# Optimization experiments

Measured on AMD Instinct MI355X. Metric: run time of the kernel, lower is better.

The kernel has to match this reference:

```python
import jax, jax.numpy as jnp
import numpy as np

D = 512        # model_size
HID = 2048     # hidden_size
NH = 8         # n_head
DH = D // NH   # head dim
L = 6          # n_layer
V = 32000      # vocab (input_size == output_size)
B, S, T = 8, 512, 512
PAD = 0
EPS = 1e-5


def setup_inputs() -> dict:
    key = jax.random.key(0)
    ks = jax.random.split(key, 16)
    sc = 0.02
    W = lambda k, shape: (jax.random.normal(k, shape) * sc).astype(jnp.float32)
    # LayerNorm params: [L, n_ln, 2, D] with [...,0,:]=gamma(ones), [...,1,:]=beta(zeros)
    ln = lambda n: jnp.stack([jnp.ones((L, n, D)), jnp.zeros((L, n, D))], axis=2)
    emi = W(ks[2], (V, D)).at[PAD].set(0.0)  # padding_idx row zeroed
    emo = W(ks[3], (V, D)).at[PAD].set(0.0)
    return {
        # token ids in [1, V) so no padding rows (avoids fully-masked softmax rows -> nan grads)
        "inputs": jax.random.randint(ks[0], (B, S), 1, V),
        "outputs": jax.random.randint(ks[1], (B, T), 1, V),
        "emi": emi, "emo": emo,
        "enc_attn_w": W(ks[4], (L, 4, D, D)), "enc_attn_b": jnp.zeros((L, 4, D)),
        "enc_ln": ln(2),
        "enc_ffn_w1": W(ks[5], (L, D, HID)), "enc_ffn_b1": jnp.zeros((L, HID)),
        "enc_ffn_w2": W(ks[6], (L, HID, D)), "enc_ffn_b2": jnp.zeros((L, D)),
        "dec_self_w": W(ks[7], (L, 4, D, D)), "dec_self_b": jnp.zeros((L, 4, D)),
        "dec_cross_w": W(ks[8], (L, 4, D, D)), "dec_cross_b": jnp.zeros((L, 4, D)),
        "dec_ln": ln(3),
        "dec_ffn_w1": W(ks[9], (L, D, HID)), "dec_ffn_b1": jnp.zeros((L, HID)),
        "dec_ffn_w2": W(ks[10], (L, HID, D)), "dec_ffn_b2": jnp.zeros((L, D)),
    }


def _ln(x, g, b):
    mu = x.mean(-1, keepdims=True)
    var = ((x - mu) ** 2).mean(-1, keepdims=True)
    return (x - mu) * jax.lax.rsqrt(var + EPS) * g + b


def _mha(xq, xkv, mask, w, b):
    # w: [4, D, D] stored as [in, out] (q, k, v, out proj); mask: [B, Sq, Sk] bool (True = masked)
    heads = lambda x: x.reshape(x.shape[0], x.shape[1], NH, DH).transpose(0, 2, 1, 3)
    q = heads(xq @ w[0] + b[0])
    k = heads(xkv @ w[1] + b[1])
    v = heads(xkv @ w[2] + b[2])
    s = jnp.einsum('bhqd,bhkd->bhqk', q, k) * (1.0 / np.sqrt(DH))
    s = jnp.where(mask[:, None], -jnp.inf, s)
    a = jnp.nan_to_num(jax.nn.softmax(s, axis=-1), nan=0.0)  # fully-masked rows -> 0
    o = jnp.einsum('bhqk,bhkd->bhqd', a, v).transpose(0, 2, 1, 3).reshape(xq.shape)
    return o @ w[3] + b[3]


def _pe(n):
    pos = jnp.arange(n, dtype=jnp.float32)[:, None]
    div = jnp.exp(jnp.arange(0, D, 2, dtype=jnp.float32) * (-np.log(10000.0) / D))
    pe = jnp.zeros((n, D))
    return pe.at[:, 0::2].set(jnp.sin(pos * div)).at[:, 1::2].set(jnp.cos(pos * div))


def reference(inputs, outputs, emi, emo,
              enc_attn_w, enc_attn_b, enc_ln, enc_ffn_w1, enc_ffn_b1, enc_ffn_w2, enc_ffn_b2,
              dec_self_w, dec_self_b, dec_cross_w, dec_cross_b, dec_ln,
              dec_ffn_w1, dec_ffn_b1, dec_ffn_w2, dec_ffn_b2):
    mx = inputs == PAD   # [B, S]
    my = outputs == PAD  # [B, T]
    x = emi[inputs] + _pe(inputs.shape[-1])
    y = emo[outputs] + _pe(outputs.shape[-1])

    enc_mask = mx[:, :, None] | mx[:, None, :]  # [B, S, S]

    def enc_layer(x, p):
        aw, ab, ln, w1, b1, w2, b2 = p
        x = _ln(x + _mha(x, x, enc_mask, aw, ab), ln[0, 0], ln[0, 1])
        x = _ln(x + (jax.nn.relu(x @ w1 + b1) @ w2 + b2), ln[1, 0], ln[1, 1])
        return x, None

    x, _ = jax.lax.scan(enc_layer, x,
                        (enc_attn_w, enc_attn_b, enc_ln, enc_ffn_w1, enc_ffn_b1, enc_ffn_w2, enc_ffn_b2))

    n = outputs.shape[-1]
    causal = jnp.triu(jnp.ones((n, n), dtype=bool), 1)
    m1 = my[:, :, None] | my[:, None, :] | causal[None]  # self-attn: pad union + causal
    m2 = my[:, :, None] | mx[:, None, :]                  # cross-attn: query pad | key pad

    def dec_layer(y, p):
        sw, sb, cw, cb, ln, w1, b1, w2, b2 = p
        y = _ln(y + _mha(y, y, m1, sw, sb), ln[0, 0], ln[0, 1])
        y = _ln(y + _mha(y, x, m2, cw, cb), ln[1, 0], ln[1, 1])
        y = _ln(y + (jax.nn.relu(y @ w1 + b1) @ w2 + b2), ln[2, 0], ln[2, 1])
        return y, None

    y, _ = jax.lax.scan(dec_layer, y,
                        (dec_self_w, dec_self_b, dec_cross_w, dec_cross_b, dec_ln,
                         dec_ffn_w1, dec_ffn_b1, dec_ffn_w2, dec_ffn_b2))
    return y  # [B, T, D] (forward returns decoder states; self.lin is unused in forward)
```

## Files before the change

kernel.cpp:

```cpp
#include <hip/hip_runtime.h>
#include <hip/hip_bf16.h>

#define D_   512
#define HID_ 2048
#define NH_  8
#define DH_  64
#define L_   6
#define B_   8
#define S_   512
#define T_   512
#define M_   4096
#define MD_  (M_ * D_)
#define QSTR 1536

typedef unsigned short ushort_t;
typedef __attribute__((ext_vector_type(8))) short bf16x8;
typedef __attribute__((ext_vector_type(4))) float f32x4;

__device__ __forceinline__ float bf2f(unsigned short u) {
    union { unsigned int i; float f; } x; x.i = ((unsigned int)u) << 16; return x.f;
}
__device__ __forceinline__ unsigned short f2bf(float f) {
    union { float f; unsigned int u; } x; x.f = f;
    unsigned int r = (x.u + 0x7fffu + ((x.u >> 16) & 1u)) >> 16;
    return (unsigned short)r;
}
__device__ __forceinline__ float ldp(const void* p, size_t i, int mode) {
    return mode ? ((const float*)p)[i] : bf2f(((const unsigned short*)p)[i]);
}

typedef __attribute__((address_space(1))) const unsigned int GAS_u32;
typedef __attribute__((address_space(3))) unsigned int LAS_u32;
__device__ __forceinline__ void gload16(const void* g, void* l) {
    __builtin_amdgcn_global_load_lds((GAS_u32*)g, (LAS_u32*)l, 16, 0, 0);
}

__global__ __launch_bounds__(256) void detect_kernel(const void* em, int* flagp) {
    __shared__ int big, zc;
    if (threadIdx.x == 0) { big = 0; zc = 0; }
    __syncthreads();
    const unsigned short* u = (const unsigned short*)em;
    int lbig = 0, lzc = 0;
    for (int i = threadIdx.x; i < 2048; i += 256) {
        unsigned short x = u[512 + i];
        float v = bf2f(x);
        if (!(fabsf(v) < 1000.0f)) lbig = 1;
        if ((((512 + i) & 1) == 0) && ((x & 0x7fff) == 0)) lzc++;
    }
    if (lbig) atomicOr(&big, 1);
    atomicAdd(&zc, lzc);
    __syncthreads();
    if (threadIdx.x == 0) flagp[0] = (big || zc >= 1000) ? 1 : 0;
}

__global__ __launch_bounds__(256) void embed_pe_kernel(const int* __restrict__ tok,
        const void* __restrict__ em, float* __restrict__ out,
        unsigned short* __restrict__ outb, const int* __restrict__ flagp)
{
    const int mode = flagp[0];
    int idx = blockIdx.x * 256 + threadIdx.x;
    int d   = idx & (D_ - 1);
    int row = idx >> 9;
    int s   = row & (S_ - 1);
    int t   = tok[row];
    float e = ldp(em, (size_t)t * D_ + d, mode);
    int d2  = d & ~1;
    float div = expf((float)d2 * (-9.210340371976184f / (float)D_));
    float a   = (float)s * div;
    float pe  = (d & 1) ? cosf(a) : sinf(a);
    float v   = e + pe;
    out[idx]  = v;
    outb[idx] = f2bf(v);
}

template<int TMT, int TNT>
__global__ __launch_bounds__(256) void mfma_gemm(
        const unsigned short* __restrict__ A, int K,
        const void* __restrict__ W, size_t woff, int nsub,
        const void* __restrict__ bias, size_t boff,
        void* __restrict__ C, int ldc, int cmode , int relu,
        const int* __restrict__ flagp)
{
    constexpr int TM  = TMT * 32;
    constexpr int TN  = TNT * 32;
    constexpr int AI  = TM / 16;
    constexpr int TPN = TN / 2;
    constexpr int KR  = TN / 16;

    __shared__ unsigned short As[TM * 32];
    __shared__ unsigned short Bs[TN * 40];

    const int mode = __builtin_amdgcn_readfirstlane(flagp[0]);
    const int tid  = threadIdx.x;
    const int m0   = blockIdx.y * TM;
    const int n0   = blockIdx.x * TN;

    const size_t wbase = woff + (size_t)(n0 / nsub) * (size_t)K * nsub + (n0 % nsub);

    const int lane = tid & 63;
    const int wave = tid >> 6;

    const int n0t = 2 * (tid % TPN);
    const int kb  = KR * (tid / TPN);

    const int ln = lane & 15;
    const int q  = lane >> 4;
    const int wm = (wave >> 1) * (TMT * 16);
    const int wn = (wave & 1) * (TNT * 16);

    f32x4 acc[TMT][TNT];
#pragma unroll
    for (int i = 0; i < TMT; ++i)
#pragma unroll
        for (int j = 0; j < TNT; ++j) acc[i][j] = (f32x4)0.0f;

    for (int k0 = 0; k0 < K; k0 += 32) {
        __syncthreads();
#pragma unroll
        for (int u = 0; u < (AI + 3) / 4; ++u) {
            int i = wave + u * 4;
            if (i < AI) {
                int off = i * 1024 + lane * 16;
                int row = off >> 6;
                int ke  = (off & 63) >> 1;
                gload16(A + (size_t)(m0 + row) * K + k0 + ke, &As[i * 512]);
            }
        }
        {
            unsigned short lo[KR], hi[KR];
            if (mode == 0) {
                const unsigned short* wp = (const unsigned short*)W + wbase;
#pragma unroll
                for (int r = 0; r < KR; ++r) {
                    unsigned int v = *reinterpret_cast<const unsigned int*>(
                        wp + (size_t)(k0 + kb + r) * nsub + n0t);
                    lo[r] = (unsigned short)(v & 0xffffu);
                    hi[r] = (unsigned short)(v >> 16);
                }
            } else {
                const float* wp = (const float*)W + wbase;
#pragma unroll
                for (int r = 0; r < KR; ++r) {
                    float2 f = *reinterpret_cast<const float2*>(
                        wp + (size_t)(k0 + kb + r) * nsub + n0t);
                    lo[r] = f2bf(f.x); hi[r] = f2bf(f.y);
                }
            }
            unsigned int ul[KR / 2], uh[KR / 2];
#pragma unroll
            for (int p = 0; p < KR / 2; ++p) {
                ul[p] = (unsigned int)lo[2 * p] | ((unsigned int)lo[2 * p + 1] << 16);
                uh[p] = (unsigned int)hi[2 * p] | ((unsigned int)hi[2 * p + 1] << 16);
            }
            if constexpr (KR == 8) {
                *reinterpret_cast<uint4*>(&Bs[(n0t + 0) * 40 + kb]) = make_uint4(ul[0], ul[1], ul[2], ul[3]);
                *reinterpret_cast<uint4*>(&Bs[(n0t + 1) * 40 + kb]) = make_uint4(uh[0], uh[1], uh[2], uh[3]);
            } else if constexpr (KR == 4) {
                *reinterpret_cast<uint2*>(&Bs[(n0t + 0) * 40 + kb]) = make_uint2(ul[0], ul[1]);
                *reinterpret_cast<uint2*>(&Bs[(n0t + 1) * 40 + kb]) = make_uint2(uh[0], uh[1]);
            } else {
                *reinterpret_cast<unsigned int*>(&Bs[(n0t + 0) * 40 + kb]) = ul[0];
                *reinterpret_cast<unsigned int*>(&Bs[(n0t + 1) * 40 + kb]) = uh[0];
            }
        }
        __syncthreads();

        bf16x8 af[TMT], bfv[TNT];
#pragma unroll
        for (int i = 0; i < TMT; ++i)
            af[i] = *reinterpret_cast<const bf16x8*>(&As[(wm + i * 16 + ln) * 32 + q * 8]);
#pragma unroll
        for (int j = 0; j < TNT; ++j)
            bfv[j] = *reinterpret_cast<const bf16x8*>(&Bs[(wn + j * 16 + ln) * 40 + q * 8]);
#pragma unroll
        for (int i = 0; i < TMT; ++i)
#pragma unroll
            for (int j = 0; j < TNT; ++j)
                acc[i][j] = __builtin_amdgcn_mfma_f32_16x16x32_bf16(af[i], bfv[j], acc[i][j], 0, 0, 0);
    }

    float bj[TNT];
#pragma unroll
    for (int j = 0; j < TNT; ++j)
        bj[j] = ldp(bias, boff + (size_t)n0 + wn + j * 16 + ln, mode);
#pragma unroll
    for (int i = 0; i < TMT; ++i) {
#pragma unroll
        for (int j = 0; j < TNT; ++j) {
            int n = n0 + wn + j * 16 + ln;
#pragma unroll
            for (int r = 0; r < 4; ++r) {
                int m = m0 + wm + i * 16 + q * 4 + r;
                float v = acc[i][j][r] + bj[j];
                if (relu) v = fmaxf(v, 0.0f);
                if (cmode == 0) ((float*)C)[(size_t)m * ldc + n] = v;
                else            ((unsigned short*)C)[(size_t)m * ldc + n] = f2bf(v);
            }
        }
    }
}

#define LSTR 68
__global__ __launch_bounds__(256) void fattn_kernel(const unsigned short* __restrict__ QKV,
        const int* __restrict__ kv_tok, unsigned short* __restrict__ O,
        int Sk, int causal)
{
    __shared__ float Qs[64 * LSTR];
    __shared__ float KVs[64 * LSTR];
    __shared__ float Ps[64 * LSTR];
    int tid = threadIdx.x;
    int bid = blockIdx.x;
    int tq = bid & 7;
    int h  = (bid >> 3) & 7;
    int b  = bid >> 6;
    int q0 = tq * 64;
    const int qg = tid >> 4, kg = tid & 15;
    const int sr = tid >> 2, sc0 = (tid & 3) * 16;

    {
        const unsigned short* p = QKV + (size_t)(b * 512 + q0 + sr) * QSTR + h * DH_ + sc0;
        uint4 u0 = *reinterpret_cast<const uint4*>(p);
        uint4 u1 = *reinterpret_cast<const uint4*>(p + 8);
        unsigned int w[8] = {u0.x, u0.y, u0.z, u0.w, u1.x, u1.y, u1.z, u1.w};
#pragma unroll
        for (int e = 0; e < 8; ++e) {
            Qs[(sc0 + 2 * e + 0) * LSTR + sr] = bf2f((unsigned short)(w[e] & 0xffffu));
            Qs[(sc0 + 2 * e + 1) * LSTR + sr] = bf2f((unsigned short)(w[e] >> 16));
        }
    }

    float m[4], l[4], o[4][4];
#pragma unroll
    for (int i = 0; i < 4; ++i) {
        m[i] = -INFINITY; l[i] = 0.0f;
#pragma unroll
        for (int j = 0; j < 4; ++j) o[i][j] = 0.0f;
    }

    const int nkt = causal ? (tq + 1) : (Sk >> 6);
    for (int kt = 0; kt < nkt; ++kt) {
        int k0 = kt * 64;
        __syncthreads();
        {
            const unsigned short* p = QKV + (size_t)(b * Sk + k0 + sr) * QSTR + 512 + h * DH_ + sc0;
            uint4 u0 = *reinterpret_cast<const uint4*>(p);
            uint4 u1 = *reinterpret_cast<const uint4*>(p + 8);
            unsigned int w[8] = {u0.x, u0.y, u0.z, u0.w, u1.x, u1.y, u1.z, u1.w};
#pragma unroll
            for (int e = 0; e < 8; ++e) {
                KVs[(sc0 + 2 * e + 0) * LSTR + sr] = bf2f((unsigned short)(w[e] & 0xffffu));
                KVs[(sc0 + 2 * e + 1) * LSTR + sr] = bf2f((unsigned short)(w[e] >> 16));
            }
        }
        __syncthreads();

        float s[4][4] = {};
        for (int d = 0; d < 64; ++d) {
            float4 a4 = *reinterpret_cast<const float4*>(&Qs[d * LSTR + qg * 4]);
            float4 b4 = *reinterpret_cast<const float4*>(&KVs[d * LSTR + kg * 4]);
            float a[4] = {a4.x, a4.y, a4.z, a4.w};
            float bb[4] = {b4.x, b4.y, b4.z, b4.w};
#pragma unroll
            for (int i = 0; i < 4; ++i)
#pragma unroll
                for (int j = 0; j < 4; ++j)
                    s[i][j] = fmaf(a[i], bb[j], s[i][j]);
        }

        int kbase = k0 + kg * 4;
        int tk[4];
#pragma unroll
        for (int j = 0; j < 4; ++j) tk[j] = kv_tok[b * Sk + kbase + j];
#pragma unroll
        for (int i = 0; i < 4; ++i) {
            int qrow = q0 + qg * 4 + i;
#pragma unroll
            for (int j = 0; j < 4; ++j) {
                bool masked = (causal && (kbase + j > qrow)) || (tk[j] == 0);
                s[i][j] = masked ? -INFINITY : s[i][j] * 0.125f;
            }
        }

#pragma unroll
        for (int i = 0; i < 4; ++i) {
            float tm = fmaxf(fmaxf(s[i][0], s[i][1]), fmaxf(s[i][2], s[i][3]));
            tm = fmaxf(tm, __shfl_xor(tm, 1, 16));
            tm = fmaxf(tm, __shfl_xor(tm, 2, 16));
            tm = fmaxf(tm, __shfl_xor(tm, 4, 16));
            tm = fmaxf(tm, __shfl_xor(tm, 8, 16));
            float mnew = fmaxf(m[i], tm);
            float alpha = (mnew == -INFINITY) ? 1.0f : __expf(m[i] - mnew);
            float p[4];
#pragma unroll
            for (int j = 0; j < 4; ++j)
                p[j] = (s[i][j] == -INFINITY) ? 0.0f : __expf(s[i][j] - mnew);
            float4 p4; p4.x = p[0]; p4.y = p[1]; p4.z = p[2]; p4.w = p[3];
            *reinterpret_cast<float4*>(&Ps[(qg * 4 + i) * LSTR + kg * 4]) = p4;
            float rs = p[0] + p[1] + p[2] + p[3];
            rs += __shfl_xor(rs, 1, 16);
            rs += __shfl_xor(rs, 2, 16);
            rs += __shfl_xor(rs, 4, 16);
            rs += __shfl_xor(rs, 8, 16);
            l[i] = l[i] * alpha + rs;
            m[i] = mnew;
#pragma unroll
            for (int j = 0; j < 4; ++j) o[i][j] *= alpha;
        }
        __syncthreads();

        {
            const unsigned short* p = QKV + (size_t)(b * Sk + k0 + sr) * QSTR + 1024 + h * DH_ + sc0;
            uint4 u0 = *reinterpret_cast<const uint4*>(p);
            uint4 u1 = *reinterpret_cast<const uint4*>(p + 8);
            unsigned int w[8] = {u0.x, u0.y, u0.z, u0.w, u1.x, u1.y, u1.z, u1.w};
#pragma unroll
            for (int e = 0; e < 8; ++e) {
                KVs[sr * LSTR + sc0 + 2 * e + 0] = bf2f((unsigned short)(w[e] & 0xffffu));
                KVs[sr * LSTR + sc0 + 2 * e + 1] = bf2f((unsigned short)(w[e] >> 16));
            }
        }
        __syncthreads();

        for (int k = 0; k < 64; ++k) {
            float4 v4 = *reinterpret_cast<const float4*>(&KVs[k * LSTR + kg * 4]);
            float vv[4] = {v4.x, v4.y, v4.z, v4.w};
            float p0 = Ps[(qg * 4 + 0) * LSTR + k];
            float p1 = Ps[(qg * 4 + 1) * LSTR + k];
            float p2 = Ps[(qg * 4 + 2) * LSTR + k];
            float p3 = Ps[(qg * 4 + 3) * LSTR + k];
#pragma unroll
            for (int j = 0; j < 4; ++j) {
                o[0][j] = fmaf(p0, vv[j], o[0][j]);
                o[1][j] = fmaf(p1, vv[j], o[1][j]);
                o[2][j] = fmaf(p2, vv[j], o[2][j]);
                o[3][j] = fmaf(p3, vv[j], o[3][j]);
            }
        }
    }

#pragma unroll
    for (int i = 0; i < 4; ++i) {
        float inv = (l[i] > 0.0f) ? 1.0f / l[i] : 0.0f;
        ushort4 r;
        r.x = f2bf(o[i][0] * inv); r.y = f2bf(o[i][1] * inv);
        r.z = f2bf(o[i][2] * inv); r.w = f2bf(o[i][3] * inv);
        *reinterpret_cast<ushort4*>(
            &O[(size_t)(b * 512 + q0 + qg * 4 + i) * D_ + h * DH_ + kg * 4]) = r;
    }
}

__global__ __launch_bounds__(256) void add_ln_kernel(float* __restrict__ X,
        unsigned short* __restrict__ Xb,
        const float* __restrict__ R, const void* __restrict__ ln, size_t goff,
        const int* __restrict__ flagp)
{
    const int mode = flagp[0];
    __shared__ float red[256];
    int row = blockIdx.x, tid = threadIdx.x;
    size_t base = (size_t)row * D_;
    float v0 = X[base + tid] + R[base + tid];
    float v1 = X[base + 256 + tid] + R[base + 256 + tid];
    red[tid] = v0 + v1; __syncthreads();
    for (int o = 128; o > 0; o >>= 1) {
        if (tid < o) red[tid] += red[tid + o];
        __syncthreads();
    }
    float mu = red[0] * (1.0f / (float)D_);
    __syncthreads();
    float d0 = v0 - mu, d1 = v1 - mu;
    red[tid] = d0 * d0 + d1 * d1; __syncthreads();
    for (int o = 128; o > 0; o >>= 1) {
        if (tid < o) red[tid] += red[tid + o];
        __syncthreads();
    }
    float inv = rsqrtf(red[0] * (1.0f / (float)D_) + 1e-5f);
    float r0 = d0 * inv * ldp(ln, goff + tid, mode)       + ldp(ln, goff + D_ + tid, mode);
    float r1 = d1 * inv * ldp(ln, goff + 256 + tid, mode) + ldp(ln, goff + D_ + 256 + tid, mode);
    X[base + tid] = r0;         Xb[base + tid] = f2bf(r0);
    X[base + 256 + tid] = r1;   Xb[base + 256 + tid] = f2bf(r1);
}

__global__ __launch_bounds__(256) void to_out_kernel(const float* __restrict__ in,
        void* __restrict__ out, int n, const int* __restrict__ flagp)
{
    const int mode = flagp[0];
    int i = blockIdx.x * 256 + threadIdx.x;
    if (i < n) {
        float v = in[i];
        if (mode) ((float*)out)[i] = v;
        else      ((__hip_bfloat16*)out)[i] = __float2bfloat16(v);
    }
}

extern "C" void kernel_launch(void* const* d_in, const int* in_sizes, int n_in,
                              void* d_out, int out_size, void* d_ws, size_t ws_size,
                              hipStream_t stream) {
    const int* tin  = (const int*)d_in[0];
    const int* tout = (const int*)d_in[1];
    const void* emi = d_in[2];
    const void* emo = d_in[3];
    const void* eaw = d_in[4];
    const void* eab = d_in[5];
    const void* eln = d_in[6];
    const void* ew1 = d_in[7];
    const void* eb1 = d_in[8];
    const void* ew2 = d_in[9];
    const void* eb2 = d_in[10];
    const void* dsw = d_in[11];
    const void* dsb = d_in[12];
    const void* dcw = d_in[13];
    const void* dcb = d_in[14];
    const void* dln = d_in[15];
    const void* dw1 = d_in[16];
    const void* db1 = d_in[17];
    const void* dw2 = d_in[18];
    const void* db2 = d_in[19];

    int*   flagp = (int*)d_ws;
    float* X = (float*)d_ws + 64;
    float* Y = X + MD_;
    float* P = Y + MD_;
    unsigned short* Xb   = (unsigned short*)(P + MD_);
    unsigned short* Yb   = Xb + MD_;
    unsigned short* QKVb = Yb + MD_;
    unsigned short* CTXb = QKVb + 3 * (size_t)MD_;
    unsigned short* HB   = QKVb;

    const size_t WDD = (size_t)D_ * D_;
    const int AGRID = B_ * NH_ * 8;

    auto g = [&](const unsigned short* A, int K, const void* W, size_t woff, int nsub,
                 const void* bias, size_t boff, void* C, int ldc, int N, int cmode, int relu) {
        mfma_gemm<1, 2><<<dim3(N / 64, M_ / 32), 256, 0, stream>>>(
            A, K, W, woff, nsub, bias, boff, C, ldc, cmode, relu, flagp);
    };

    detect_kernel<<<1, 256, 0, stream>>>(emi, flagp);
    embed_pe_kernel<<<(M_ * D_) / 256, 256, 0, stream>>>(tin, emi, X, Xb, flagp);
    embed_pe_kernel<<<(M_ * D_) / 256, 256, 0, stream>>>(tout, emo, Y, Yb, flagp);

    for (int l = 0; l < L_; ++l) {
        size_t w = (size_t)l * 4 * WDD, bb = (size_t)l * 4 * D_;
        g(Xb, D_, eaw, w, 512, eab, bb, QKVb, QSTR, 1536, 1, 0);
        fattn_kernel<<<AGRID, 256, 0, stream>>>(QKVb, tin, CTXb, S_, 0);
        g(CTXb, D_, eaw, w + 3 * WDD, 512, eab, bb + 3 * D_, P, D_, 512, 0, 0);
        add_ln_kernel<<<M_, 256, 0, stream>>>(X, Xb, P, eln, ((size_t)l * 2 + 0) * 2 * D_, flagp);
        g(Xb, D_, ew1, (size_t)l * D_ * HID_, 2048, eb1, (size_t)l * HID_, HB, HID_, 2048, 1, 1);
        g(HB, HID_, ew2, (size_t)l * HID_ * D_, 512, eb2, (size_t)l * D_, P, D_, 512, 0, 0);
        add_ln_kernel<<<M_, 256, 0, stream>>>(X, Xb, P, eln, ((size_t)l * 2 + 1) * 2 * D_, flagp);
    }

    for (int l = 0; l < L_; ++l) {
        size_t w = (size_t)l * 4 * WDD, bb = (size_t)l * 4 * D_;
        g(Yb, D_, dsw, w, 512, dsb, bb, QKVb, QSTR, 1536, 1, 0);
        fattn_kernel<<<AGRID, 256, 0, stream>>>(QKVb, tout, CTXb, T_, 1);
        g(CTXb, D_, dsw, w + 3 * WDD, 512, dsb, bb + 3 * D_, P, D_, 512, 0, 0);
        add_ln_kernel<<<M_, 256, 0, stream>>>(Y, Yb, P, dln, ((size_t)l * 3 + 0) * 2 * D_, flagp);
        g(Yb, D_, dcw, w, 512, dcb, bb, QKVb, QSTR, 512, 1, 0);
        g(Xb, D_, dcw, w + WDD, 512, dcb, bb + D_, QKVb + 512, QSTR, 1024, 1, 0);
        fattn_kernel<<<AGRID, 256, 0, stream>>>(QKVb, tin, CTXb, S_, 0);
        g(CTXb, D_, dcw, w + 3 * WDD, 512, dcb, bb + 3 * D_, P, D_, 512, 0, 0);
        add_ln_kernel<<<M_, 256, 0, stream>>>(Y, Yb, P, dln, ((size_t)l * 3 + 1) * 2 * D_, flagp);
        g(Yb, D_, dw1, (size_t)l * D_ * HID_, 2048, db1, (size_t)l * HID_, HB, HID_, 2048, 1, 1);
        g(HB, HID_, dw2, (size_t)l * HID_ * D_, 512, db2, (size_t)l * D_, P, D_, 512, 0, 0);
        add_ln_kernel<<<M_, 256, 0, stream>>>(Y, Yb, P, dln, ((size_t)l * 3 + 2) * 2 * D_, flagp);
    }

    to_out_kernel<<<(out_size + 255) / 256, 256, 0, stream>>>(Y, d_out, out_size, flagp);
}
```

Measured before the change: 4.138 ms.

## Rewrite flash attention kernel with bf16 MFMA and swizzled LDS tiles

Replaces the scalar fp32 FMA attention kernel with one where each wave computes a 16-row query slice using 16x16x32 bf16 MFMA instructions for both QK^T and PV. Q, K, transposed V and P are kept in LDS as bf16 with an XOR swizzle to avoid bank conflicts, and the extra barrier between softmax and the V load is removed. The aim is to move attention math onto the matrix cores and cut LDS traffic. The risk is a small precision change, because P is rounded to bf16 before the PV product.

```diff
diff --git a/kernel.cpp b/kernel.cpp
--- a/kernel.cpp
+++ b/kernel.cpp
@@ -200,152 +200,156 @@
     }
 }
 
-#define LSTR 68
+__device__ __forceinline__ bf16x8 lds_frag(const unsigned short* base, int row, int slot) {
+    return *reinterpret_cast<const bf16x8*>(
+        (const char*)base + row * 128 + ((slot ^ (row & 7)) << 4));
+}
+
 __global__ __launch_bounds__(256) void fattn_kernel(const unsigned short* __restrict__ QKV,
         const int* __restrict__ kv_tok, unsigned short* __restrict__ O,
         int Sk, int causal)
 {
-    __shared__ float Qs[64 * LSTR];
-    __shared__ float KVs[64 * LSTR];
-    __shared__ float Ps[64 * LSTR];
-    int tid = threadIdx.x;
-    int bid = blockIdx.x;
-    int tq = bid & 7;
-    int h  = (bid >> 3) & 7;
-    int b  = bid >> 6;
-    int q0 = tq * 64;
-    const int qg = tid >> 4, kg = tid & 15;
-    const int sr = tid >> 2, sc0 = (tid & 3) * 16;
+    __shared__ unsigned short Qs[64 * 64];
+    __shared__ unsigned short Ks[64 * 64];
+    __shared__ unsigned short Vt[64 * 64];
+    __shared__ unsigned short Ps[64 * 64];
+
+    const int tid = threadIdx.x;
+    const int bid = blockIdx.x;
+    const int tq = bid & 7;
+    const int h  = (bid >> 3) & 7;
+    const int b  = bid >> 6;
+    const int q0 = tq * 64;
+
+    const int lane = tid & 63;
+    const int wave = tid >> 6;
+    const int ln   = lane & 15;
+    const int g    = lane >> 4;
+
+    const int srow = tid & 63;
+    const int sslc = tid >> 6;
 
     {
-        const unsigned short* p = QKV + (size_t)(b * 512 + q0 + sr) * QSTR + h * DH_ + sc0;
-        uint4 u0 = *reinterpret_cast<const uint4*>(p);
-        uint4 u1 = *reinterpret_cast<const uint4*>(p + 8);
-        unsigned int w[8] = {u0.x, u0.y, u0.z, u0.w, u1.x, u1.y, u1.z, u1.w};
-#pragma unroll
-        for (int e = 0; e < 8; ++e) {
-            Qs[(sc0 + 2 * e + 0) * LSTR + sr] = bf2f((unsigned short)(w[e] & 0xffffu));
-            Qs[(sc0 + 2 * e + 1) * LSTR + sr] = bf2f((unsigned short)(w[e] >> 16));
-        }
-    }
-
-    float m[4], l[4], o[4][4];
-#pragma unroll
-    for (int i = 0; i < 4; ++i) {
-        m[i] = -INFINITY; l[i] = 0.0f;
-#pragma unroll
-        for (int j = 0; j < 4; ++j) o[i][j] = 0.0f;
-    }
+        const unsigned short* qp = QKV + (size_t)(b * 512 + q0 + srow) * QSTR + h * DH_;
+#pragma unroll
+        for (int it = 0; it < 2; ++it) {
+            int sl = sslc + it * 4;
+            uint4 v = *reinterpret_cast<const uint4*>(qp + sl * 8);
+            *reinterpret_cast<uint4*>((char*)Qs + srow * 128 + ((sl ^ (srow & 7)) << 4)) = v;
+        }
+    }
+
+    float mrow[4], lrow[4];
+    f32x4 o[4];
+#pragma unroll
+    for (int r = 0; r < 4; ++r) { mrow[r] = -INFINITY; lrow[r] = 0.0f; }
+#pragma unroll
+    for (int j = 0; j < 4; ++j) o[j] = (f32x4)0.0f;
 
     const int nkt = causal ? (tq + 1) : (Sk >> 6);
     for (int kt = 0; kt < nkt; ++kt) {
-        int k0 = kt * 64;
+        const int k0 = kt * 64;
         __syncthreads();
         {
-            const unsigned short* p = QKV + (size_t)(b * Sk + k0 + sr) * QSTR + 512 + h * DH_ + sc0;
-            uint4 u0 = *reinterpret_cast<const uint4*>(p);
-            uint4 u1 = *reinterpret_cast<const uint4*>(p + 8);
-            unsigned int w[8] = {u0.x, u0.y, u0.z, u0.w, u1.x, u1.y, u1.z, u1.w};
-#pragma unroll
-            for (int e = 0; e < 8; ++e) {
-                KVs[(sc0 + 2 * e + 0) * LSTR + sr] = bf2f((unsigned short)(w[e] & 0xffffu));
-                KVs[(sc0 + 2 * e + 1) * LSTR + sr] = bf2f((unsigned short)(w[e] >> 16));
-            }
-        }
-        __syncthreads();
-
-        float s[4][4] = {};
-        for (int d = 0; d < 64; ++d) {
-            float4 a4 = *reinterpret_cast<const float4*>(&Qs[d * LSTR + qg * 4]);
-            float4 b4 = *reinterpret_cast<const float4*>(&KVs[d * LSTR + kg * 4]);
-            float a[4] = {a4.x, a4.y, a4.z, a4.w};
-            float bb[4] = {b4.x, b4.y, b4.z, b4.w};
-#pragma unroll
-            for (int i = 0; i < 4; ++i)
-#pragma unroll
-                for (int j = 0; j < 4; ++j)
-                    s[i][j] = fmaf(a[i], bb[j], s[i][j]);
-        }
-
-        int kbase = k0 + kg * 4;
+            const unsigned short* kp = QKV + (size_t)(b * Sk + k0 + srow) * QSTR + 512  + h * DH_;
+            const unsigned short* vp = QKV + (size_t)(b * Sk + k0 + srow) * QSTR + 1024 + h * DH_;
+#pragma unroll
+            for (int it = 0; it < 2; ++it) {
+                int sl = sslc + it * 4;
+                uint4 kv = *reinterpret_cast<const uint4*>(kp + sl * 8);
+                *reinterpret_cast<uint4*>((char*)Ks + srow * 128 + ((sl ^ (srow & 7)) << 4)) = kv;
+                uint4 vv = *reinterpret_cast<const uint4*>(vp + sl * 8);
+                unsigned int w[4] = {vv.x, vv.y, vv.z, vv.w};
+#pragma unroll
+                for (int e = 0; e < 8; ++e) {
+                    int d = sl * 8 + e;
+                    unsigned short val = (e & 1) ? (unsigned short)(w[e >> 1] >> 16)
+                                                 : (unsigned short)(w[e >> 1] & 0xffffu);
+                    *(unsigned short*)((char*)Vt + d * 128 + (((srow >> 3) ^ (d & 7)) << 4)
+                                       + (srow & 7) * 2) = val;
+                }
+            }
+        }
+        __syncthreads();
+
+        f32x4 s[4];
+#pragma unroll
+        for (int j = 0; j < 4; ++j) s[j] = (f32x4)0.0f;
+        __builtin_amdgcn_s_setprio(1);
+#pragma unroll
+        for (int ks = 0; ks < 2; ++ks) {
+            bf16x8 qf = lds_frag(Qs, wave * 16 + ln, g + ks * 4);
+#pragma unroll
+            for (int j = 0; j < 4; ++j) {
+                bf16x8 kf = lds_frag(Ks, j * 16 + ln, g + ks * 4);
+                s[j] = __builtin_amdgcn_mfma_f32_16x16x32_bf16(qf, kf, s[j], 0, 0, 0);
+            }
+        }
+        __builtin_amdgcn_s_setprio(0);
+
         int tk[4];
 #pragma unroll
-        for (int j = 0; j < 4; ++j) tk[j] = kv_tok[b * Sk + kbase + j];
-#pragma unroll
-        for (int i = 0; i < 4; ++i) {
-            int qrow = q0 + qg * 4 + i;
+        for (int j = 0; j < 4; ++j) tk[j] = kv_tok[b * Sk + k0 + j * 16 + ln];
+
+#pragma unroll
+        for (int r = 0; r < 4; ++r) {
+            const int qrow = q0 + wave * 16 + g * 4 + r;
+            float sv[4];
 #pragma unroll
             for (int j = 0; j < 4; ++j) {
-                bool masked = (causal && (kbase + j > qrow)) || (tk[j] == 0);
-                s[i][j] = masked ? -INFINITY : s[i][j] * 0.125f;
-            }
-        }
-
-#pragma unroll
-        for (int i = 0; i < 4; ++i) {
-            float tm = fmaxf(fmaxf(s[i][0], s[i][1]), fmaxf(s[i][2], s[i][3]));
+                bool masked = (causal && (k0 + j * 16 + ln > qrow)) || (tk[j] == 0);
+                sv[j] = masked ? -INFINITY : s[j][r] * 0.125f;
+            }
+            float tm = fmaxf(fmaxf(sv[0], sv[1]), fmaxf(sv[2], sv[3]));
             tm = fmaxf(tm, __shfl_xor(tm, 1, 16));
             tm = fmaxf(tm, __shfl_xor(tm, 2, 16));
             tm = fmaxf(tm, __shfl_xor(tm, 4, 16));
             tm = fmaxf(tm, __shfl_xor(tm, 8, 16));
-            float mnew = fmaxf(m[i], tm);
-            float alpha = (mnew == -INFINITY) ? 1.0f : __expf(m[i] - mnew);
-            float p[4];
-#pragma unroll
-            for (int j = 0; j < 4; ++j)
-                p[j] = (s[i][j] == -INFINITY) ? 0.0f : __expf(s[i][j] - mnew);
-            float4 p4; p4.x = p[0]; p4.y = p[1]; p4.z = p[2]; p4.w = p[3];
-            *reinterpret_cast<float4*>(&Ps[(qg * 4 + i) * LSTR + kg * 4]) = p4;
-            float rs = p[0] + p[1] + p[2] + p[3];
+            float mnew = fmaxf(mrow[r], tm);
+            float alpha = (mnew == -INFINITY) ? 1.0f : __expf(mrow[r] - mnew);
+            float p[4], rs = 0.0f;
+#pragma unroll
+            for (int j = 0; j < 4; ++j) {
+                p[j] = (sv[j] == -INFINITY) ? 0.0f : __expf(sv[j] - mnew);
+                rs += p[j];
+            }
             rs += __shfl_xor(rs, 1, 16);
             rs += __shfl_xor(rs, 2, 16);
             rs += __shfl_xor(rs, 4, 16);
             rs += __shfl_xor(rs, 8, 16);
-            l[i] = l[i] * alpha + rs;
-            m[i] = mnew;
-#pragma unroll
-            for (int j = 0; j < 4; ++j) o[i][j] *= alpha;
-        }
-        __syncthreads();
-
-        {
-            const unsigned short* p = QKV + (size_t)(b * Sk + k0 + sr) * QSTR + 1024 + h * DH_ + sc0;
-            uint4 u0 = *reinterpret_cast<const uint4*>(p);
-            uint4 u1 = *reinterpret_cast<const uint4*>(p + 8);
-            unsigned int w[8] = {u0.x, u0.y, u0.z, u0.w, u1.x, u1.y, u1.z, u1.w};
-#pragma unroll
-            for (int e = 0; e < 8; ++e) {
-                KVs[sr * LSTR + sc0 + 2 * e + 0] = bf2f((unsigned short)(w[e] & 0xffffu));
-                KVs[sr * LSTR + sc0 + 2 * e + 1] = bf2f((unsigned short)(w[e] >> 16));
-            }
-        }
-        __syncthreads();
-
-        for (int k = 0; k < 64; ++k) {
-            float4 v4 = *reinterpret_cast<const float4*>(&KVs[k * LSTR + kg * 4]);
-            float vv[4] = {v4.x, v4.y, v4.z, v4.w};
-            float p0 = Ps[(qg * 4 + 0) * LSTR + k];
-            float p1 = Ps[(qg * 4 + 1) * LSTR + k];
-            float p2 = Ps[(qg * 4 + 2) * LSTR + k];
-            float p3 = Ps[(qg * 4 + 3) * LSTR + k];
+            lrow[r] = lrow[r] * alpha + rs;
+            mrow[r] = mnew;
+#pragma unroll
+            for (int j = 0; j < 4; ++j) o[j][r] *= alpha;
+            const int prow = wave * 16 + g * 4 + r;
 #pragma unroll
             for (int j = 0; j < 4; ++j) {
-                o[0][j] = fmaf(p0, vv[j], o[0][j]);
-                o[1][j] = fmaf(p1, vv[j], o[1][j]);
-                o[2][j] = fmaf(p2, vv[j], o[2][j]);
-                o[3][j] = fmaf(p3, vv[j], o[3][j]);
-            }
-        }
-    }
-
-#pragma unroll
-    for (int i = 0; i < 4; ++i) {
-        float inv = (l[i] > 0.0f) ? 1.0f / l[i] : 0.0f;
-        ushort4 r;
-        r.x = f2bf(o[i][0] * inv); r.y = f2bf(o[i][1] * inv);
-        r.z = f2bf(o[i][2] * inv); r.w = f2bf(o[i][3] * inv);
-        *reinterpret_cast<ushort4*>(
-            &O[(size_t)(b * 512 + q0 + qg * 4 + i) * D_ + h * DH_ + kg * 4]) = r;
+                int col = j * 16 + ln;
+                *(unsigned short*)((char*)Ps + prow * 128 + ((((col >> 3) ^ (prow & 7))) << 4)
+                                   + (col & 7) * 2) = f2bf(p[j]);
+            }
+        }
+
+        __builtin_amdgcn_s_setprio(1);
+#pragma unroll
+        for (int ks = 0; ks < 2; ++ks) {
+            bf16x8 pf = lds_frag(Ps, wave * 16 + ln, g + ks * 4);
+#pragma unroll
+            for (int j = 0; j < 4; ++j) {
+                bf16x8 vf = lds_frag(Vt, j * 16 + ln, g + ks * 4);
+                o[j] = __builtin_amdgcn_mfma_f32_16x16x32_bf16(pf, vf, o[j], 0, 0, 0);
+            }
+        }
+        __builtin_amdgcn_s_setprio(0);
+    }
+
+#pragma unroll
+    for (int r = 0; r < 4; ++r) {
+        float inv = (lrow[r] > 0.0f) ? 1.0f / lrow[r] : 0.0f;
+        int qrow = q0 + wave * 16 + g * 4 + r;
+#pragma unroll
+        for (int j = 0; j < 4; ++j)
+            O[(size_t)(b * 512 + qrow) * D_ + h * DH_ + j * 16 + ln] = f2bf(o[j][r] * inv);
     }
 }
 
```

Result: faster. 3.350 ms (-19.0%).
